# Kernel tuning notes

Hardware: AMD Instinct MI355X
Metric: run time of the kernel (lower is better)

## Reference

```python
import jax, jax.numpy as jnp
import numpy as np

NUM_HEADS = 8
EPS = 1e-3

N_TOKENS = 32768
DIM = 256
N_WIN = 128
WIN = N_TOKENS // N_WIN  # 256 tokens per window


def setup_inputs() -> dict:
    key = jax.random.key(0)
    ks = jax.random.split(key, 4)
    x = jax.random.normal(ks[0], (N_TOKENS, DIM), dtype=jnp.float32)
    # torch nn.Linear weights are [out_features, in_features]
    w_qkv = jax.random.normal(ks[1], (3 * DIM, DIM), dtype=jnp.float32) * (DIM ** -0.5)
    w_proj = jax.random.normal(ks[2], (DIM, DIM), dtype=jnp.float32) * (DIM ** -0.5)
    b_proj = jnp.zeros((DIM,), dtype=jnp.float32)
    batch_win_inds = (jnp.arange(N_TOKENS) // WIN).astype(jnp.int64)
    offsets = (jnp.arange(N_WIN) * WIN).astype(jnp.int64)
    counts = jnp.full((N_WIN,), WIN, dtype=jnp.int64)
    return {"x": x, "w_qkv": w_qkv, "w_proj": w_proj, "b_proj": b_proj,
            "offsets": offsets, "counts": counts, "batch_win_inds": batch_win_inds}


def reference(x, w_qkv, w_proj, b_proj, offsets, counts, batch_win_inds):
    N, C = x.shape
    H = NUM_HEADS
    hd = C // H
    W = counts.shape[0]  # number of windows (static)

    qkv = x @ w_qkv.T                      # [N, 3C]
    q, k, v = jnp.split(qkv, 3, axis=-1)   # each [N, C]
    q = jax.nn.relu(q.reshape(N, H, hd))   # [N, H, hd]
    k = jax.nn.relu(k.reshape(N, H, hd))
    v = v.reshape(N, H, hd)

    seg = batch_win_inds.astype(jnp.int32)
    # per-window KV state: kv[w] = sum_{i in w} k_i^T v_i   -> [W, H, hd, hd]
    kv = jax.ops.segment_sum(jnp.einsum('nhc,nhd->nhcd', k, v), seg, num_segments=W)
    # per-window key sum for normalizer                      -> [W, H, hd]
    s = jax.ops.segment_sum(k, seg, num_segments=W)

    y = jnp.einsum('nhc,nhcd->nhd', q, kv[seg])              # [N, H, hd]
    z = jnp.sum(s[seg] * q, axis=-1, keepdims=True)          # [N, H, 1]
    y = y / (z + EPS)

    y = y.reshape(N, C) @ w_proj.T + b_proj                  # [N, C]
    return y
```

## Files before the change

kernel.cpp:

```cpp
#include <hip/hip_runtime.h>

typedef __bf16 bf16_t;
typedef bf16_t bf16x8 __attribute__((ext_vector_type(8)));
typedef bf16_t bf16x4 __attribute__((ext_vector_type(4)));
typedef float f32x4 __attribute__((ext_vector_type(4)));

#define M_TOK 32768
#define NWIN 128
#define WIN  256

typedef __attribute__((address_space(3))) void* as3p;
typedef const __attribute__((address_space(1))) void* as1p;

__device__ __forceinline__ void gll16(const void* g, void* l) {
    __builtin_amdgcn_global_load_lds((as1p)g, (as3p)l, 16, 0, 0);
}

#define VMW_(n) asm volatile("s_waitcnt vmcnt(" #n ")" ::: "memory")
#define VMW(n) VMW_(n)

#define MFMA16(b, a, c) __builtin_amdgcn_mfma_f32_16x16x32_bf16((b), (a), (c), 0, 0, 0)

__global__ __launch_bounds__(256) void wconv(
    const float* __restrict__ wq, const float* __restrict__ wp,
    bf16_t* __restrict__ wqb, bf16_t* __restrict__ wpb)
{
    int i4 = (blockIdx.x * 256 + threadIdx.x) * 4;
    const float* s; bf16_t* dst; int idx;
    if (i4 < 196608) { s = wq; dst = wqb; idx = i4; }
    else             { s = wp; dst = wpb; idx = i4 - 196608; }
    f32x4 v = *(const f32x4*)(s + idx);
    bf16x4 o;
    o[0] = (bf16_t)v[0]; o[1] = (bf16_t)v[1]; o[2] = (bf16_t)v[2]; o[3] = (bf16_t)v[3];
    *(bf16x4*)(dst + idx) = o;
}

__global__ __launch_bounds__(512) void fused_attn(
    const float* __restrict__ X,
    const bf16_t* __restrict__ Wq,
    const int* __restrict__ offsets,
    const int* __restrict__ counts,
    bf16_t* __restrict__ Y)
{
    __shared__ __align__(16) bf16_t Xb[65536];
    __shared__ __align__(16) bf16_t SCR[16384];

    const int bid = blockIdx.x;
    const int w  = (bid & 7) * 16 + (bid >> 4);
    const int hh = (bid >> 3) & 1;
    const int is64 = (counts[1] == 0) ? 1 : 0;
    const int off = offsets[w << is64];
    const int tid = threadIdx.x;
    const int lane = tid & 63;
    const int wv = tid >> 6;
    const int r = lane & 15, q = lane >> 4;

    bf16_t* Wl  = SCR;
    bf16_t* KT  = SCR;
    bf16_t* VT  = SCR + 8192;
    bf16_t* Ql  = SCR;
    bf16_t* kvb = SCR + 10240;
    float*  sfp = (float*)(SCR + 11264);
    float*  zin = (float*)(SCR + 11328);

#pragma unroll 8
    for (int it = 0; it < 32; ++it) {
        const int L = it * 512 + tid;
        const int row = L >> 6, col4 = L & 63;
        f32x4 v = *(const f32x4*)(X + (size_t)(off + row) * 256 + col4 * 4);
        bf16x4 o;
        o[0] = (bf16_t)v[0]; o[1] = (bf16_t)v[1]; o[2] = (bf16_t)v[2]; o[3] = (bf16_t)v[3];
        const int gs = (col4 >> 1) ^ (row & 7);
        *(bf16x4*)(Xb + row * 256 + gs * 8 + (col4 & 1) * 4) = o;
    }
    __syncthreads();

    for (int h4 = 0; h4 < 4; ++h4) {
        const int h = hh * 4 + h4;

#pragma unroll
        for (int u = 0; u < 4; ++u) {
            const int rowl = wv * 8 + u * 2 + (lane >> 5);
            const size_t grow = (size_t)((wv < 4 ? 256 : 480) + h * 32 + rowl);
            gll16(Wq + grow * 256 + ((lane & 31) ^ (rowl & 7)) * 8,
                  Wl + (wv * 8 + u * 2) * 256);
        }
        __syncthreads();

        f32x4 aQ[2][2] = {}, aK[2][2] = {}, aV[2][2] = {};
#pragma unroll
        for (int kch = 0; kch < 8; ++kch) {
            const int slot8 = (((kch * 4 + q) ^ (r & 7)) * 8);
            bf16x8 xa[2];
#pragma unroll
            for (int i2 = 0; i2 < 2; ++i2)
                xa[i2] = *(const bf16x8*)(Xb + (wv * 32 + i2 * 16 + r) * 256 + slot8);
#pragma unroll
            for (int ct = 0; ct < 2; ++ct) {
                bf16x8 bq = *(const bf16x8*)(Wq + (size_t)(h * 32 + ct * 16 + r) * 256
                                              + kch * 32 + q * 8);
                bf16x8 bk = *(const bf16x8*)(Wl + (ct * 16 + r) * 256 + slot8);
                bf16x8 bv = *(const bf16x8*)(Wl + (32 + ct * 16 + r) * 256 + slot8);
#pragma unroll
                for (int i2 = 0; i2 < 2; ++i2) {
                    aQ[i2][ct] = MFMA16(bq, xa[i2], aQ[i2][ct]);
                    aK[i2][ct] = MFMA16(bk, xa[i2], aK[i2][ct]);
                    aV[i2][ct] = MFMA16(bv, xa[i2], aV[i2][ct]);
                }
            }
        }
        __syncthreads();

#pragma unroll
        for (int i2 = 0; i2 < 2; ++i2) {
            const int t = wv * 32 + i2 * 16 + r;
            const int gt = t >> 3;
#pragma unroll
            for (int ct = 0; ct < 2; ++ct)
#pragma unroll
                for (int reg = 0; reg < 4; ++reg) {
                    const int c = ct * 16 + q * 4 + reg;
                    const int ei = c * 256 + (gt ^ (c & 7)) * 8 + (t & 7);
                    KT[ei] = (bf16_t)fmaxf(aK[i2][ct][reg], 0.f);
                    VT[ei] = (bf16_t)aV[i2][ct][reg];
                }
        }
        __syncthreads();

        f32x4 kva = {};
        float sc = 0.f;
        if (wv < 4) {
            const int ct = wv >> 1, dt = wv & 1;
#pragma unroll
            for (int kch = 0; kch < 8; ++kch) {
                const int slot8 = (((kch * 4 + q) ^ (r & 7)) * 8);
                bf16x8 ak = *(const bf16x8*)(KT + (ct * 16 + r) * 256 + slot8);
                bf16x8 bv = *(const bf16x8*)(VT + (dt * 16 + r) * 256 + slot8);
                kva = MFMA16(bv, ak, kva);
            }
        } else {
            const int tl = tid - 256;
            const int c = tl >> 3, p = tl & 7;
#pragma unroll
            for (int g = 0; g < 4; ++g) {
                bf16x8 kk = *(const bf16x8*)(KT + c * 256 + (p + g * 8) * 8);
#pragma unroll
                for (int j = 0; j < 8; ++j) sc += (float)kk[j];
            }
            sc += __shfl_xor(sc, 1);
            sc += __shfl_xor(sc, 2);
            sc += __shfl_xor(sc, 4);
        }
        __syncthreads();

#pragma unroll
        for (int i2 = 0; i2 < 2; ++i2) {
            const int t = wv * 32 + i2 * 16 + r;
#pragma unroll
            for (int ct = 0; ct < 2; ++ct) {
                bf16x4 o;
#pragma unroll
                for (int reg = 0; reg < 4; ++reg)
                    o[reg] = (bf16_t)fmaxf(aQ[i2][ct][reg], 0.f);
                *(bf16x4*)(Ql + t * 40 + ct * 16 + q * 4) = o;
            }
        }
        if (wv < 4) {
            const int ct = wv >> 1, dt = wv & 1;
#pragma unroll
            for (int reg = 0; reg < 4; ++reg)
                kvb[(dt * 16 + q * 4 + reg) * 32 + ct * 16 + r] = (bf16_t)kva[reg];
        } else {
            const int tl = tid - 256;
            if ((tl & 7) == 0) sfp[tl >> 3] = sc;
        }
        __syncthreads();

        if (tid < 256) {
            float z = 0.f;
#pragma unroll
            for (int g = 0; g < 4; ++g) {
                bf16x8 qq = *(const bf16x8*)(Ql + tid * 40 + g * 8);
#pragma unroll
                for (int j = 0; j < 8; ++j) z += (float)qq[j] * sfp[g * 8 + j];
            }
            zin[tid] = 1.f / (z + 1e-3f);
        }
        __syncthreads();

        {
            bf16x8 bk0 = *(const bf16x8*)(kvb + r * 32 + q * 8);
            bf16x8 bk1 = *(const bf16x8*)(kvb + (16 + r) * 32 + q * 8);
#pragma unroll
            for (int i2 = 0; i2 < 2; ++i2) {
                const int t = wv * 32 + i2 * 16 + r;
                bf16x8 aq = *(const bf16x8*)(Ql + t * 40 + q * 8);
                f32x4 y0 = {}, y1 = {};
                y0 = MFMA16(bk0, aq, y0);
                y1 = MFMA16(bk1, aq, y1);
                const float zi = zin[t];
                bf16x4 o0, o1;
#pragma unroll
                for (int reg = 0; reg < 4; ++reg) {
                    o0[reg] = (bf16_t)(y0[reg] * zi);
                    o1[reg] = (bf16_t)(y1[reg] * zi);
                }
                bf16_t* yp = Y + (size_t)(off + t) * 256 + h * 32;
                *(bf16x4*)(yp + q * 4) = o0;
                *(bf16x4*)(yp + 16 + q * 4) = o1;
            }
        }
        __syncthreads();
    }
}

__global__ __launch_bounds__(512) void gemm2_proj(
    const bf16_t* __restrict__ Y,
    const bf16_t* __restrict__ Wb,
    const float* __restrict__ bias,
    float* __restrict__ Out)
{
    __shared__ __align__(16) bf16_t Al[64][256];
    __shared__ __align__(16) bf16_t Bs[3][128][64];

    const int tid = threadIdx.x;
    const int lane = tid & 63;
    const int wv = tid >> 6;
    const int wm = wv >> 2, wn = wv & 3;
    const int m0 = blockIdx.x * 64;
    const int r = lane & 15, q = lane >> 4;
    const int rl = lane >> 3, gsl = lane & 7;

    f32x4 acc[2][2] = {};

    auto stageB = [&](int t) {
        const int nb = t >> 2, kc = (t & 3) * 64;
#pragma unroll
        for (int u = 0; u < 2; ++u)
            gll16(Wb + (size_t)(nb * 128 + wv * 16 + u * 8 + rl) * 256 + kc + (gsl ^ rl) * 8,
                  &Bs[t % 3][wv * 16 + u * 8][0]);
    };

    auto comp = [&](int t) {
        const int buf = t % 3;
#pragma unroll
        for (int s = 0; s < 2; ++s) {
            const int kk = (t & 3) * 2 + s;
            bf16x8 a[2], b[2];
#pragma unroll
            for (int i = 0; i < 2; ++i)
                a[i] = *(const bf16x8*)((const bf16_t*)Al +
                        (wm * 32 + i * 16 + r) * 256 + ((kk * 4 + q) ^ (r & 7)) * 8);
#pragma unroll
            for (int j = 0; j < 2; ++j)
                b[j] = *(const bf16x8*)&Bs[buf][wn * 32 + j * 16 + r][((s * 4 + q) ^ (r & 7)) * 8];
#pragma unroll
            for (int i = 0; i < 2; ++i)
#pragma unroll
                for (int j = 0; j < 2; ++j)
                    acc[i][j] = MFMA16(b[j], a[i], acc[i][j]);
        }
    };

    auto wout = [&](int nb) {
#pragma unroll
        for (int i = 0; i < 2; ++i) {
            const int rowg = m0 + wm * 32 + i * 16 + r;
#pragma unroll
            for (int j = 0; j < 2; ++j) {
                const int n = nb * 128 + wn * 32 + j * 16 + q * 4;
                f32x4 bi = *(const f32x4*)(bias + n);
                f32x4 o;
#pragma unroll
                for (int reg = 0; reg < 4; ++reg) o[reg] = acc[i][j][reg] + bi[reg];
                *(f32x4*)&Out[(size_t)rowg * 256 + n] = o;
                acc[i][j] = (f32x4){0.f, 0.f, 0.f, 0.f};
            }
        }
    };

#pragma unroll
    for (int u = 0; u < 4; ++u) {
        const int rowl = wv * 8 + u * 2 + (lane >> 5);
        const int gsrc = (lane & 31) ^ (rowl & 7);
        gll16(Y + (size_t)(m0 + rowl) * 256 + gsrc * 8, &Al[wv * 8 + u * 2][0]);
    }
    stageB(0); stageB(1); stageB(2);

#define G2S(t, NW) do { \
        VMW(NW); \
        __builtin_amdgcn_s_barrier(); \
        __builtin_amdgcn_sched_barrier(0); \
        comp(t); \
        if (((t) & 3) == 3) wout((t) >> 2); \
        __builtin_amdgcn_sched_barrier(0); \
        __builtin_amdgcn_s_barrier(); \
        if ((t) + 3 < 8) stageB((t) + 3); \
    } while (0)

    G2S(0, 4); G2S(1, 4); G2S(2, 4); G2S(3, 4);
    G2S(4, 4); G2S(5, 4); G2S(6, 2); G2S(7, 0);
#undef G2S
}

extern "C" void kernel_launch(void* const* d_in, const int* in_sizes, int n_in,
                              void* d_out, int out_size, void* d_ws, size_t ws_size,
                              hipStream_t stream) {
    const float* x      = (const float*)d_in[0];
    const float* w_qkv  = (const float*)d_in[1];
    const float* w_proj = (const float*)d_in[2];
    const float* b_proj = (const float*)d_in[3];
    const int*   offs   = (const int*)d_in[4];
    const int*   cnts   = (const int*)d_in[5];

    char* ws = (char*)d_ws;
    bf16_t* Y   = (bf16_t*)(ws + 50331648);
    bf16_t* Wqb = (bf16_t*)(ws + 67108864);
    bf16_t* Wpb = (bf16_t*)(ws + 67502080);
    float*  out = (float*)d_out;

    wconv<<<256, 256, 0, stream>>>(w_qkv, w_proj, Wqb, Wpb);

    fused_attn<<<256, 512, 0, stream>>>(x, Wqb, offs, cnts, Y);

    gemm2_proj<<<512, 512, 0, stream>>>(Y, Wpb, b_proj, out);
}
```

Before: 133.2 us.

## Keep X in registers, double-buffer QKV weights in LDS, trim barriers

X rows are loaded straight from global into registers as bf16 MFMA fragments rather than staged through a 128KB LDS tile. The Q, K and V weight slices for each head are now all staged in LDS and double-buffered, so the next head's weights are prefetched during the current head's compute. Several __syncthreads are replaced with lgkmcnt waits plus raw barriers, and some are removed by giving each buffer its own LDS region. This cuts LDS footprint and serialization and adds a global-to-LDS prefetch overlap, at the cost of more register pressure from holding 16 bf16x8 X fragments.

After: 129.6 us. -2.7%, faster.

```diff
diff --git a/kernel.cpp b/kernel.cpp
--- a/kernel.cpp
+++ b/kernel.cpp
@@ -16,8 +16,16 @@
     __builtin_amdgcn_global_load_lds((as1p)g, (as3p)l, 16, 0, 0);
 }
 
+__device__ __forceinline__ bf16x8 cvt8(f32x4 a, f32x4 b) {
+    bf16x8 o;
+    o[0] = (bf16_t)a[0]; o[1] = (bf16_t)a[1]; o[2] = (bf16_t)a[2]; o[3] = (bf16_t)a[3];
+    o[4] = (bf16_t)b[0]; o[5] = (bf16_t)b[1]; o[6] = (bf16_t)b[2]; o[7] = (bf16_t)b[3];
+    return o;
+}
+
 #define VMW_(n) asm volatile("s_waitcnt vmcnt(" #n ")" ::: "memory")
 #define VMW(n) VMW_(n)
+#define LGKM0 asm volatile("s_waitcnt lgkmcnt(0)" ::: "memory")
 
 #define MFMA16(b, a, c) __builtin_amdgcn_mfma_f32_16x16x32_bf16((b), (a), (c), 0, 0, 0)
 
@@ -42,8 +50,13 @@
     const int* __restrict__ counts,
     bf16_t* __restrict__ Y)
 {
-    __shared__ __align__(16) bf16_t Xb[65536];
-    __shared__ __align__(16) bf16_t SCR[16384];
+    __shared__ __align__(16) bf16_t Wl2[2][96 * 256];
+    __shared__ __align__(16) bf16_t KT[32 * 256];
+    __shared__ __align__(16) bf16_t VT[32 * 256];
+    __shared__ __align__(16) bf16_t Ql[256 * 40];
+    __shared__ __align__(16) bf16_t kvb[32 * 32];
+    __shared__ float sfp[32];
+    __shared__ float zin[256];
 
     const int bid = blockIdx.x;
     const int w  = (bid & 7) * 16 + (bid >> 4);
@@ -55,61 +68,55 @@
     const int wv = tid >> 6;
     const int r = lane & 15, q = lane >> 4;
 
-    bf16_t* Wl  = SCR;
-    bf16_t* KT  = SCR;
-    bf16_t* VT  = SCR + 8192;
-    bf16_t* Ql  = SCR;
-    bf16_t* kvb = SCR + 10240;
-    float*  sfp = (float*)(SCR + 11264);
-    float*  zin = (float*)(SCR + 11328);
-
-#pragma unroll 8
-    for (int it = 0; it < 32; ++it) {
-        const int L = it * 512 + tid;
-        const int row = L >> 6, col4 = L & 63;
-        f32x4 v = *(const f32x4*)(X + (size_t)(off + row) * 256 + col4 * 4);
-        bf16x4 o;
-        o[0] = (bf16_t)v[0]; o[1] = (bf16_t)v[1]; o[2] = (bf16_t)v[2]; o[3] = (bf16_t)v[3];
-        const int gs = (col4 >> 1) ^ (row & 7);
-        *(bf16x4*)(Xb + row * 256 + gs * 8 + (col4 & 1) * 4) = o;
+    auto stageW = [&](int h, int buf) {
+#pragma unroll
+        for (int u = 0; u < 6; ++u) {
+            const int rl = wv * 12 + u * 2 + (lane >> 5);
+            const int grow = (rl < 32 ? 256 + rl : (rl < 64 ? 480 + rl : rl - 64)) + h * 32;
+            gll16(Wq + (size_t)grow * 256 + ((lane & 31) ^ (rl & 7)) * 8,
+                  &Wl2[buf][(wv * 12 + u * 2) * 256]);
+        }
+    };
+
+    stageW(hh * 4, 0);
+    bf16x8 xr[2][8];
+#pragma unroll
+    for (int i2 = 0; i2 < 2; ++i2) {
+        const float* xp = X + (size_t)(off + wv * 32 + i2 * 16 + r) * 256 + q * 8;
+#pragma unroll
+        for (int kch = 0; kch < 8; ++kch) {
+            f32x4 lo = *(const f32x4*)(xp + kch * 32);
+            f32x4 hi = *(const f32x4*)(xp + kch * 32 + 4);
+            xr[i2][kch] = cvt8(lo, hi);
+        }
     }
-    __syncthreads();
 
     for (int h4 = 0; h4 < 4; ++h4) {
         const int h = hh * 4 + h4;
-
-#pragma unroll
-        for (int u = 0; u < 4; ++u) {
-            const int rowl = wv * 8 + u * 2 + (lane >> 5);
-            const size_t grow = (size_t)((wv < 4 ? 256 : 480) + h * 32 + rowl);
-            gll16(Wq + grow * 256 + ((lane & 31) ^ (rowl & 7)) * 8,
-                  Wl + (wv * 8 + u * 2) * 256);
-        }
-        __syncthreads();
+        const int buf = h4 & 1;
+        VMW(0);
+        __builtin_amdgcn_s_barrier();
+        __builtin_amdgcn_sched_barrier(0);
+        const bf16_t* Wl = &Wl2[buf][0];
 
         f32x4 aQ[2][2] = {}, aK[2][2] = {}, aV[2][2] = {};
 #pragma unroll
         for (int kch = 0; kch < 8; ++kch) {
             const int slot8 = (((kch * 4 + q) ^ (r & 7)) * 8);
-            bf16x8 xa[2];
-#pragma unroll
-            for (int i2 = 0; i2 < 2; ++i2)
-                xa[i2] = *(const bf16x8*)(Xb + (wv * 32 + i2 * 16 + r) * 256 + slot8);
 #pragma unroll
             for (int ct = 0; ct < 2; ++ct) {
-                bf16x8 bq = *(const bf16x8*)(Wq + (size_t)(h * 32 + ct * 16 + r) * 256
-                                              + kch * 32 + q * 8);
                 bf16x8 bk = *(const bf16x8*)(Wl + (ct * 16 + r) * 256 + slot8);
                 bf16x8 bv = *(const bf16x8*)(Wl + (32 + ct * 16 + r) * 256 + slot8);
+                bf16x8 bq = *(const bf16x8*)(Wl + (64 + ct * 16 + r) * 256 + slot8);
 #pragma unroll
                 for (int i2 = 0; i2 < 2; ++i2) {
-                    aQ[i2][ct] = MFMA16(bq, xa[i2], aQ[i2][ct]);
-                    aK[i2][ct] = MFMA16(bk, xa[i2], aK[i2][ct]);
-                    aV[i2][ct] = MFMA16(bv, xa[i2], aV[i2][ct]);
+                    aQ[i2][ct] = MFMA16(bq, xr[i2][kch], aQ[i2][ct]);
+                    aK[i2][ct] = MFMA16(bk, xr[i2][kch], aK[i2][ct]);
+                    aV[i2][ct] = MFMA16(bv, xr[i2][kch], aV[i2][ct]);
                 }
             }
         }
-        __syncthreads();
+        if (h4 < 3) stageW(h + 1, buf ^ 1);
 
 #pragma unroll
         for (int i2 = 0; i2 < 2; ++i2) {
@@ -125,7 +132,9 @@
                     VT[ei] = (bf16_t)aV[i2][ct][reg];
                 }
         }
-        __syncthreads();
+        LGKM0;
+        __builtin_amdgcn_s_barrier();
+        __builtin_amdgcn_sched_barrier(0);
 
         f32x4 kva = {};
         float sc = 0.f;
@@ -135,8 +144,8 @@
             for (int kch = 0; kch < 8; ++kch) {
                 const int slot8 = (((kch * 4 + q) ^ (r & 7)) * 8);
                 bf16x8 ak = *(const bf16x8*)(KT + (ct * 16 + r) * 256 + slot8);
-                bf16x8 bv = *(const bf16x8*)(VT + (dt * 16 + r) * 256 + slot8);
-                kva = MFMA16(bv, ak, kva);
+                bf16x8 bv2 = *(const bf16x8*)(VT + (dt * 16 + r) * 256 + slot8);
+                kva = MFMA16(bv2, ak, kva);
             }
         } else {
             const int tl = tid - 256;
@@ -151,7 +160,6 @@
             sc += __shfl_xor(sc, 2);
             sc += __shfl_xor(sc, 4);
         }
-        __syncthreads();
 
 #pragma unroll
         for (int i2 = 0; i2 < 2; ++i2) {
@@ -174,7 +182,9 @@
             const int tl = tid - 256;
             if ((tl & 7) == 0) sfp[tl >> 3] = sc;
         }
-        __syncthreads();
+        LGKM0;
+        __builtin_amdgcn_s_barrier();
+        __builtin_amdgcn_sched_barrier(0);
 
         if (tid < 256) {
             float z = 0.f;
@@ -186,7 +196,9 @@
             }
             zin[tid] = 1.f / (z + 1e-3f);
         }
-        __syncthreads();
+        LGKM0;
+        __builtin_amdgcn_s_barrier();
+        __builtin_amdgcn_sched_barrier(0);
 
         {
             bf16x8 bk0 = *(const bf16x8*)(kvb + r * 32 + q * 8);
@@ -210,7 +222,6 @@
                 *(bf16x4*)(yp + 16 + q * 4) = o1;
             }
         }
-        __syncthreads();
     }
 }
 
```
